# Performance work log

Hardware: AMD Instinct MI355X
Metric: run time of the kernel (lower is better)

Reference implementation:

```python
import jax, jax.numpy as jnp
import numpy as np

N, E, G = 50000, 1600000, 500
H, F, NG, L, OUT = 128, 128, 50, 6, 1
LOG2 = float(np.log(2.0))

def ssp(x):
    return jax.nn.softplus(x) - LOG2

def setup_inputs() -> dict:
    key = jax.random.key(0)
    ks = jax.random.split(key, 16)
    inp = {
        'z': jax.random.randint(ks[0], (N,), 0, 100),
        'pos': jax.random.normal(ks[1], (N, 3), jnp.float32) * 5.0,
        'batch': jnp.sort(jax.random.randint(ks[2], (N,), 0, G)),
        'edge_index': jax.random.randint(ks[3], (2, E), 0, N),
        # parameters
        'emb': jax.random.normal(ks[4], (100, H), jnp.float32) * 0.1,
        'dist_W': jax.random.normal(ks[5], (1, NG), jnp.float32) * 0.1,
        'dist_b': jnp.zeros((NG,), jnp.float32),
        'Wn': jax.random.normal(ks[6], (L, H, F), jnp.float32) * (1.0 / np.sqrt(H)),
        'We': jax.random.normal(ks[7], (L, NG, F), jnp.float32) * (1.0 / np.sqrt(NG)),
        'be': jnp.zeros((L, F), jnp.float32),
        'Wo': jax.random.normal(ks[8], (L, F, H), jnp.float32) * (1.0 / np.sqrt(F)),
        'bo': jnp.zeros((L, H), jnp.float32),
        'W1': jax.random.normal(ks[9], (H, H // 2), jnp.float32) * (1.0 / np.sqrt(H)),
        'b1': jnp.zeros((H // 2,), jnp.float32),
        'W2': jax.random.normal(ks[10], (H // 2, OUT), jnp.float32) * (1.0 / np.sqrt(H // 2)),
        'b2': jnp.zeros((OUT,), jnp.float32),
    }
    return inp

def reference(z, pos, batch, edge_index, emb, dist_W, dist_b, Wn, We, be, Wo, bo, W1, b1, W2, b2):
    row, col = edge_index[0], edge_index[1]
    # edge distances -> Linear(1, num_gaussians)
    dist = jnp.linalg.norm(pos[row] - pos[col], axis=-1)            # [E]
    e = dist[:, None] * dist_W[0][None, :] + dist_b                 # [E, NG]
    v = emb[z]                                                      # [N, H]
    # edge-conditioned message passing x num_layers
    for i in range(Wn.shape[0]):
        h = v @ Wn[i]                                               # [N, F]
        msg = h[col] * (e @ We[i] + be[i])                          # [E, F]
        agg = jax.ops.segment_sum(msg, row, num_segments=v.shape[0])
        v = ssp(agg @ Wo[i] + bo[i])                                # [N, H]
    # readout
    u = ssp(v @ W1 + b1) @ W2 + b2                                  # [N, OUT]
    return jax.ops.segment_sum(u, batch, num_segments=G)            # [G, OUT]
```

## Files before the change

### kernel.cpp

```cpp
#include <hip/hip_runtime.h>
#include <math.h>

#define HDIM 128
#define NGAUSS 50
#define NLAYER 6
#define TSTR 136
#define DINV (1.0f/512.0f)
#define NXCD 8
#define NSTRIPE 512

typedef unsigned short ushortT;
typedef __attribute__((ext_vector_type(8))) short bf16x8;
typedef __attribute__((ext_vector_type(4))) float f32x4;

static __device__ __forceinline__ float bf2f(unsigned short u){
  union { unsigned int i; float f; } x; x.i = ((unsigned int)u) << 16; return x.f;
}
static __device__ __forceinline__ float bitsf(unsigned int i){
  union { unsigned int i; float f; } x; x.i = i; return x.f;
}
static __device__ __forceinline__ unsigned short f2bf(float f){
  union { float f; unsigned int i; } x; x.f = f;
  unsigned int i = x.i;
  unsigned int r = (i + 0x7FFFu + ((i >> 16) & 1u)) >> 16;
  return (unsigned short)r;
}
static __device__ __forceinline__ float ssp(float x){
  return fmaxf(x, 0.0f) + __logf(1.0f + __expf(-fabsf(x))) - 0.69314718055994530942f;
}
static __device__ __forceinline__ f32x4 mfma4r(const bf16x8* a, const bf16x8* b){
  f32x4 d = {0.f, 0.f, 0.f, 0.f};
  d = __builtin_amdgcn_mfma_f32_16x16x32_bf16(a[0], b[0], d, 0, 0, 0);
  d = __builtin_amdgcn_mfma_f32_16x16x32_bf16(a[1], b[1], d, 0, 0, 0);
  d = __builtin_amdgcn_mfma_f32_16x16x32_bf16(a[2], b[2], d, 0, 0, 0);
  d = __builtin_amdgcn_mfma_f32_16x16x32_bf16(a[3], b[3], d, 0, 0, 0);
  return d;
}


__global__ __launch_bounds__(256)
void k_hist(const int* __restrict__ erow, int* __restrict__ hist,
            int E, int NB, int shift, int estripe){
  __shared__ int lh[512];
  int tid = threadIdx.x, w = blockIdx.x;
  for (int i = tid; i < NB; i += 256) lh[i] = 0;
  __syncthreads();
  int beg = w * estripe;
  int end = beg + estripe; if (end > E) end = E;
  for (int e = beg + tid; e < end; e += 256)
    atomicAdd(&lh[erow[e] >> shift], 1);
  __syncthreads();
  for (int i = tid; i < NB; i += 256) hist[w * 512 + i] = lh[i];
}

__global__ __launch_bounds__(256)
void k_colscan(int* __restrict__ hist, int* __restrict__ colTotal, int NB){
  __shared__ int sA[512], sB[512];
  int b = blockIdx.x, tid = threadIdx.x;
  sA[tid]       = hist[tid * 512 + b];
  sA[tid + 256] = hist[(tid + 256) * 512 + b];
  __syncthreads();
  int* pa = sA; int* pb = sB;
  for (int off = 1; off < 512; off <<= 1){
    for (int i = tid; i < 512; i += 256)
      pb[i] = pa[i] + (i >= off ? pa[i - off] : 0);
    __syncthreads();
    int* t = pa; pa = pb; pb = t;
  }
  int e0 = (tid == 0) ? 0 : pa[tid - 1];
  int e1 = pa[tid + 255];
  hist[tid * 512 + b]       = e0;
  hist[(tid + 256) * 512 + b] = e1;
  if (tid == 0) colTotal[b] = pa[511];
}

__global__ __launch_bounds__(256)
void k_bscan(const int* __restrict__ colTotal, int* __restrict__ bucketBase, int NB){
  __shared__ int sA[512], sB[512];
  int tid = threadIdx.x;
  for (int i = tid; i < 512; i += 256) sA[i] = (i < NB) ? colTotal[i] : 0;
  __syncthreads();
  int* pa = sA; int* pb = sB;
  for (int off = 1; off < 512; off <<= 1){
    for (int i = tid; i < 512; i += 256)
      pb[i] = pa[i] + (i >= off ? pa[i - off] : 0);
    __syncthreads();
    int* t = pa; pa = pb; pb = t;
  }
  for (int i = tid; i < NB; i += 256)
    bucketBase[i] = (i == 0) ? 0 : pa[i - 1];
  if (tid == 0) bucketBase[NB] = pa[NB - 1];
}

__global__ __launch_bounds__(256)
void k_scatter(const int* __restrict__ erow, const int* __restrict__ ecol,
               const float* __restrict__ pos, const int* __restrict__ hist,
               const int* __restrict__ bucketBase, uint2* __restrict__ stg,
               int E, int NB, int shift, int estripe){
  __shared__ int cur[512];
  int tid = threadIdx.x, w = blockIdx.x;
  for (int b = tid; b < NB; b += 256)
    cur[b] = bucketBase[b] + hist[w * 512 + b];
  __syncthreads();
  int beg = w * estripe;
  int end = beg + estripe; if (end > E) end = E;
  int mask = (1 << shift) - 1;
  for (int e = beg + tid; e < end; e += 256){
    int r = erow[e], c = ecol[e];
    float dx = pos[r*3+0] - pos[c*3+0];
    float dy = pos[r*3+1] - pos[c*3+1];
    float dz = pos[r*3+2] - pos[c*3+2];
    float d = sqrtf(dx*dx + dy*dy + dz*dz);
    int du = (int)(d * 512.0f + 0.5f);
    if (du > 65535) du = 65535;
    int p = atomicAdd(&cur[r >> shift], 1);
    uint2 t;
    t.x = ((unsigned int)c << 16) | (unsigned int)du;
    t.y = (unsigned int)(r & mask);
    stg[p] = t;
  }
}

__global__ __launch_bounds__(256)
void k_place(const uint2* __restrict__ stg, const int* __restrict__ bucketBase,
             int* __restrict__ offsets, unsigned int* __restrict__ csr,
             int N, int NB, int shift, int E){
  __shared__ int rc[1024];
  __shared__ int sA[1024], sB[1024];
  int b = blockIdx.x, tid = threadIdx.x;
  int R = 1 << shift;
  int r0 = b << shift;
  int s = bucketBase[b], e2 = bucketBase[b + 1];
  for (int i = tid; i < R; i += 256) rc[i] = 0;
  __syncthreads();
  for (int j = s + tid; j < e2; j += 256)
    atomicAdd(&rc[stg[j].y], 1);
  __syncthreads();
  for (int i = tid; i < R; i += 256) sA[i] = rc[i];
  __syncthreads();
  int* pa = sA; int* pb = sB;
  for (int off = 1; off < R; off <<= 1){
    for (int i = tid; i < R; i += 256)
      pb[i] = pa[i] + (i >= off ? pa[i - off] : 0);
    __syncthreads();
    int* t = pa; pa = pb; pb = t;
  }
  for (int i = tid; i < R; i += 256){
    int excl = (i == 0) ? 0 : pa[i - 1];
    rc[i] = excl;
    int r = r0 + i;
    if (r < N) offsets[r] = s + excl;
  }
  if (b == NB - 1 && tid == 0) offsets[N] = E;
  __syncthreads();
  for (int j = s + tid; j < e2; j += 256){
    uint2 t = stg[j];
    int slot = s + atomicAdd(&rc[t.y], 1);
    csr[slot] = t.x;
  }
}

__global__ void k_setup(const int* __restrict__ z, const float* __restrict__ emb,
                        ushortT* __restrict__ vhi,
                        const float* __restrict__ Wn, ushortT* __restrict__ WnT,
                        const float* __restrict__ Wo, ushortT* __restrict__ WoT,
                        const float* __restrict__ dW, const float* __restrict__ db,
                        const float* __restrict__ We, const float* __restrict__ be,
                        float* __restrict__ a, float* __restrict__ c,
                        const int* __restrict__ batch, int* __restrict__ groupOff,
                        const float* __restrict__ W1, ushortT* __restrict__ W1T,
                        int N, int G, int B1, int B2, int B4, int B5, int B7){
  int b = blockIdx.x;
  int tid = threadIdx.x;
  if (b < B1){
    int idx = b * 256 + tid;
    if (idx < N * HDIM){
      int n = idx >> 7, f = idx & 127;
      vhi[idx] = f2bf(emb[z[n] * HDIM + f]);
    }
    return;
  }
  b -= B1;
  if (b < B2){
    int idx = b * 256 + tid;
    if (idx < NLAYER * HDIM * HDIM){
      int mat = idx >> 14, rem = idx & 16383;
      int n = rem >> 7, k = rem & 127;
      WnT[idx] = f2bf(Wn[(mat << 14) + k * HDIM + n]);
    }
    return;
  }
  b -= B2;
  if (b < B2){
    int idx = b * 256 + tid;
    if (idx < NLAYER * HDIM * HDIM){
      int mat = idx >> 14, rem = idx & 16383;
      int n = rem >> 7, k = rem & 127;
      WoT[idx] = f2bf(Wo[(mat << 14) + k * HDIM + n]);
    }
    return;
  }
  b -= B2;
  if (b < B4){
    int idx = b * 256 + tid;
    if (idx < NLAYER * HDIM){
      int l = idx >> 7, f = idx & 127;
      float av = 0.f, cv = 0.f;
      for (int g = 0; g < NGAUSS; ++g){
        float we = We[(l * NGAUSS + g) * HDIM + f];
        av += dW[g] * we;
        cv += db[g] * we;
      }
      a[idx] = av;
      c[idx] = cv + be[idx];
    }
    return;
  }
  b -= B4;
  if (b < B5){
    int i = b * 256 + tid;
    if (i >= N) return;
    int bb = batch[i];
    if (i == 0){
      for (int g = 0; g <= bb; ++g) groupOff[g] = 0;
    } else {
      int pb = batch[i - 1];
      for (int g = pb + 1; g <= bb; ++g) groupOff[g] = i;
    }
    if (i == N - 1){
      for (int g = bb + 1; g <= G; ++g) groupOff[g] = N;
    }
    return;
  }
  b -= B5;
  if (b < B7){
    int idx = b * 256 + tid;
    if (idx < 64 * HDIM){
      int ncol = idx >> 7, k = idx & 127;
      W1T[idx] = f2bf(W1[k * 64 + ncol]);
    }
  }
}

__global__ __launch_bounds__(128, 2)
void k_gemm0(const ushortT* __restrict__ X, const ushortT* __restrict__ WT,
             ushortT* __restrict__ outHi, int N){
  int tid = threadIdx.x;
  int wave = tid >> 6, lane = tid & 63;
  int m = lane & 15, quad = lane >> 4;
  int ntiles = (N + 15) >> 4;
  int t0 = (blockIdx.x * 2 + wave) * 2;
  if (t0 >= ntiles) return;

  bf16x8 av[2][4];
  #pragma unroll
  for (int rt = 0; rt < 2; ++rt){
    int row = (t0 + rt) * 16 + m; if (row >= N) row = N - 1;
    #pragma unroll
    for (int kk = 0; kk < 4; ++kk)
      av[rt][kk] = *(const bf16x8*)(X + ((size_t)row << 7) + kk*32 + quad*8);
  }
  #pragma unroll
  for (int ct = 0; ct < 8; ++ct){
    int ncol = ct * 16 + m;
    const ushortT* bp = WT + ((size_t)ncol << 7) + quad*8;
    bf16x8 bb[4];
    #pragma unroll
    for (int kk = 0; kk < 4; ++kk) bb[kk] = *(const bf16x8*)(bp + kk*32);
    #pragma unroll
    for (int rt = 0; rt < 2; ++rt){
      f32x4 d = mfma4r(av[rt], bb);
      #pragma unroll
      for (int r = 0; r < 4; ++r){
        int orow = (t0 + rt) * 16 + quad*4 + r;
        if (orow < N) outHi[((size_t)orow << 7) + ncol] = f2bf(d[r]);
      }
    }
  }
}

#define AGG_PROC(P, DD) do { \
    unsigned int w_; float lo_, hi_; \
    w_ = (P).x; lo_ = bitsf(w_ << 16); hi_ = bitsf(w_ & 0xFFFF0000u); \
    s1[0] = fmaf(lo_, (DD), s1[0]); s0[0] += lo_; \
    s1[1] = fmaf(hi_, (DD), s1[1]); s0[1] += hi_; \
    w_ = (P).y; lo_ = bitsf(w_ << 16); hi_ = bitsf(w_ & 0xFFFF0000u); \
    s1[2] = fmaf(lo_, (DD), s1[2]); s0[2] += lo_; \
    s1[3] = fmaf(hi_, (DD), s1[3]); s0[3] += hi_; \
    w_ = (P).z; lo_ = bitsf(w_ << 16); hi_ = bitsf(w_ & 0xFFFF0000u); \
    s1[4] = fmaf(lo_, (DD), s1[4]); s0[4] += lo_; \
    s1[5] = fmaf(hi_, (DD), s1[5]); s0[5] += hi_; \
    w_ = (P).w; lo_ = bitsf(w_ << 16); hi_ = bitsf(w_ & 0xFFFF0000u); \
    s1[6] = fmaf(lo_, (DD), s1[6]); s0[6] += lo_; \
    s1[7] = fmaf(hi_, (DD), s1[7]); s0[7] += hi_; \
  } while(0)

#define GATH(Q) (*(const uint4*)(h + ((size_t)((Q) >> 16) << 7) + fl))

__global__ __launch_bounds__(256, 6)
void k_agg2(const ushortT* __restrict__ h, const int* __restrict__ offsets,
            const unsigned int* __restrict__ cd, const float* __restrict__ a,
            const float* __restrict__ c, ushortT* __restrict__ aggHi,
            int N, int segNodes){
  int xcd = blockIdx.x & (NXCD - 1);
  int idx = blockIdx.x >> 3;
  int node = xcd * segNodes + idx * 4 + (threadIdx.x >> 6);
  if (node >= N || node >= (xcd + 1) * segNodes) return;
  int lane = threadIdx.x & 63;
  int quarter = lane >> 4;
  int fl = (lane & 15) * 8;
  int s = offsets[node], e = offsets[node + 1];
  float s0[8] = {0.f,0.f,0.f,0.f,0.f,0.f,0.f,0.f};
  float s1[8] = {0.f,0.f,0.f,0.f,0.f,0.f,0.f,0.f};
  int efull = s + ((e - s) & ~7);
  int L = s;
  if (efull - s >= 16){
    unsigned int qA0 = cd[L + quarter],      qA1 = cd[L + 4 + quarter];
    uint4 pA0 = GATH(qA0), pA1 = GATH(qA1);
    unsigned int qB0 = cd[L + 8 + quarter],  qB1 = cd[L + 12 + quarter];
    uint4 pB0 = GATH(qB0), pB1 = GATH(qB1);
    float dA0 = (float)(qA0 & 0xFFFFu) * DINV, dA1 = (float)(qA1 & 0xFFFFu) * DINV;
    float dB0 = (float)(qB0 & 0xFFFFu) * DINV, dB1 = (float)(qB1 & 0xFFFFu) * DINV;
    L += 16;
    for (; L + 16 <= efull; L += 16){
      unsigned int nA0 = cd[L + quarter], nA1 = cd[L + 4 + quarter];
      AGG_PROC(pA0, dA0); AGG_PROC(pA1, dA1);
      pA0 = GATH(nA0); pA1 = GATH(nA1);
      dA0 = (float)(nA0 & 0xFFFFu) * DINV; dA1 = (float)(nA1 & 0xFFFFu) * DINV;
      unsigned int nB0 = cd[L + 8 + quarter], nB1 = cd[L + 12 + quarter];
      AGG_PROC(pB0, dB0); AGG_PROC(pB1, dB1);
      pB0 = GATH(nB0); pB1 = GATH(nB1);
      dB0 = (float)(nB0 & 0xFFFFu) * DINV; dB1 = (float)(nB1 & 0xFFFFu) * DINV;
    }
    AGG_PROC(pA0, dA0); AGG_PROC(pA1, dA1);
    AGG_PROC(pB0, dB0); AGG_PROC(pB1, dB1);
  }
  for (; L + 8 <= efull; L += 8){
    unsigned int q0 = cd[L + quarter], q1 = cd[L + 4 + quarter];
    uint4 p0 = GATH(q0), p1 = GATH(q1);
    float d0 = (float)(q0 & 0xFFFFu) * DINV, d1 = (float)(q1 & 0xFFFFu) * DINV;
    AGG_PROC(p0, d0); AGG_PROC(p1, d1);
  }
  for (int j = efull; j < e; j += 4){
    int myj = j + quarter;
    if (myj < e){
      unsigned int q = cd[myj];
      uint4 p = GATH(q);
      float dd = (float)(q & 0xFFFFu) * DINV;
      AGG_PROC(p, dd);
    }
  }
  float4 av0 = *(const float4*)(a + fl);
  float4 av1 = *(const float4*)(a + fl + 4);
  float4 cv0 = *(const float4*)(c + fl);
  float4 cv1 = *(const float4*)(c + fl + 4);
  float r[8];
  r[0] = av0.x * s1[0] + cv0.x * s0[0];
  r[1] = av0.y * s1[1] + cv0.y * s0[1];
  r[2] = av0.z * s1[2] + cv0.z * s0[2];
  r[3] = av0.w * s1[3] + cv0.w * s0[3];
  r[4] = av1.x * s1[4] + cv1.x * s0[4];
  r[5] = av1.y * s1[5] + cv1.y * s0[5];
  r[6] = av1.z * s1[6] + cv1.z * s0[6];
  r[7] = av1.w * s1[7] + cv1.w * s0[7];
  #pragma unroll
  for (int k = 0; k < 8; ++k){
    r[k] += __shfl_down(r[k], 32, 64);
    r[k] += __shfl_down(r[k], 16, 64);
  }
  if (quarter == 0){
    uint4 st;
    st.x = (unsigned int)f2bf(r[0]) | ((unsigned int)f2bf(r[1]) << 16);
    st.y = (unsigned int)f2bf(r[2]) | ((unsigned int)f2bf(r[3]) << 16);
    st.z = (unsigned int)f2bf(r[4]) | ((unsigned int)f2bf(r[5]) << 16);
    st.w = (unsigned int)f2bf(r[6]) | ((unsigned int)f2bf(r[7]) << 16);
    *(uint4*)(aggHi + ((size_t)node << 7) + fl) = st;
  }
}

__global__ __launch_bounds__(128, 2)
void k_fpair(const ushortT* __restrict__ agg, const ushortT* __restrict__ WoT,
             const float* __restrict__ bo, const ushortT* __restrict__ WnT,
             ushortT* __restrict__ outH, int N, int segTiles){
  __shared__ ushortT vt[2][32 * TSTR];
  int tid = threadIdx.x;
  int wave = tid >> 6, lane = tid & 63;
  int m = lane & 15, quad = lane >> 4;
  int ntiles = (N + 15) >> 4;
  int xcd = blockIdx.x & (NXCD - 1);
  int idx = blockIdx.x >> 3;
  int wjIdx = idx * 2 + wave;
  int segWJ = segTiles >> 1;
  if (wjIdx >= segWJ) return;
  int t0 = xcd * segTiles + wjIdx * 2;
  if (t0 >= ntiles) return;
  ushortT* vw = vt[wave];

  bf16x8 av[2][4];
  #pragma unroll
  for (int rt = 0; rt < 2; ++rt){
    int row = (t0 + rt) * 16 + m; if (row >= N) row = N - 1;
    #pragma unroll
    for (int kk = 0; kk < 4; ++kk)
      av[rt][kk] = *(const bf16x8*)(agg + ((size_t)row << 7) + kk*32 + quad*8);
  }
  #pragma unroll
  for (int ct = 0; ct < 8; ++ct){
    int ncol = ct * 16 + m;
    const ushortT* bp = WoT + ((size_t)ncol << 7) + quad*8;
    bf16x8 bb[4];
    #pragma unroll
    for (int kk = 0; kk < 4; ++kk) bb[kk] = *(const bf16x8*)(bp + kk*32);
    float bbias = bo[ncol];
    #pragma unroll
    for (int rt = 0; rt < 2; ++rt){
      f32x4 d = mfma4r(av[rt], bb);
      #pragma unroll
      for (int r = 0; r < 4; ++r)
        vw[(rt*16 + quad*4 + r) * TSTR + ncol] = f2bf(ssp(d[r] + bbias));
    }
  }
  bf16x8 a2[2][4];
  #pragma unroll
  for (int rt = 0; rt < 2; ++rt){
    #pragma unroll
    for (int kk = 0; kk < 4; ++kk)
      a2[rt][kk] = *(const bf16x8*)(&vw[(rt*16 + m) * TSTR + kk*32 + quad*8]);
  }
  #pragma unroll
  for (int ct = 0; ct < 8; ++ct){
    int ncol = ct * 16 + m;
    const ushortT* bp = WnT + ((size_t)ncol << 7) + quad*8;
    bf16x8 bb[4];
    #pragma unroll
    for (int kk = 0; kk < 4; ++kk) bb[kk] = *(const bf16x8*)(bp + kk*32);
    #pragma unroll
    for (int rt = 0; rt < 2; ++rt){
      f32x4 d = mfma4r(a2[rt], bb);
      #pragma unroll
      for (int r = 0; r < 4; ++r){
        int orow = (t0 + rt) * 16 + quad*4 + r;
        if (orow < N) outH[((size_t)orow << 7) + ncol] = f2bf(d[r]);
      }
    }
  }
}

__global__ __launch_bounds__(128, 2)
void k_gfinal(const ushortT* __restrict__ agg, const ushortT* __restrict__ WoT,
              const float* __restrict__ bo, const ushortT* __restrict__ W1T,
              const float* __restrict__ b1, const float* __restrict__ W2,
              const float* __restrict__ b2, float* __restrict__ u,
              int N, int segTiles){
  __shared__ ushortT vt[2][32 * TSTR];
  int tid = threadIdx.x;
  int wave = tid >> 6, lane = tid & 63;
  int m = lane & 15, quad = lane >> 4;
  int ntiles = (N + 15) >> 4;
  int xcd = blockIdx.x & (NXCD - 1);
  int idx = blockIdx.x >> 3;
  int wjIdx = idx * 2 + wave;
  int segWJ = segTiles >> 1;
  if (wjIdx >= segWJ) return;
  int t0 = xcd * segTiles + wjIdx * 2;
  if (t0 >= ntiles) return;
  ushortT* vw = vt[wave];

  bf16x8 av[2][4];
  #pragma unroll
  for (int rt = 0; rt < 2; ++rt){
    int row = (t0 + rt) * 16 + m; if (row >= N) row = N - 1;
    #pragma unroll
    for (int kk = 0; kk < 4; ++kk)
      av[rt][kk] = *(const bf16x8*)(agg + ((size_t)row << 7) + kk*32 + quad*8);
  }
  #pragma unroll
  for (int ct = 0; ct < 8; ++ct){
    int ncol = ct * 16 + m;
    const ushortT* bp = WoT + ((size_t)ncol << 7) + quad*8;
    bf16x8 bb[4];
    #pragma unroll
    for (int kk = 0; kk < 4; ++kk) bb[kk] = *(const bf16x8*)(bp + kk*32);
    float bbias = bo[ncol];
    #pragma unroll
    for (int rt = 0; rt < 2; ++rt){
      f32x4 d = mfma4r(av[rt], bb);
      #pragma unroll
      for (int r = 0; r < 4; ++r)
        vw[(rt*16 + quad*4 + r) * TSTR + ncol] = f2bf(ssp(d[r] + bbias));
    }
  }
  bf16x8 a2[2][4];
  #pragma unroll
  for (int rt = 0; rt < 2; ++rt){
    #pragma unroll
    for (int kk = 0; kk < 4; ++kk)
      a2[rt][kk] = *(const bf16x8*)(&vw[(rt*16 + m) * TSTR + kk*32 + quad*8]);
  }
  float acc[2][4] = {{0.f,0.f,0.f,0.f},{0.f,0.f,0.f,0.f}};
  #pragma unroll
  for (int ct = 0; ct < 4; ++ct){
    int ncol = ct * 16 + m;
    const ushortT* bp = W1T + ((size_t)ncol << 7) + quad*8;
    bf16x8 bb[4];
    #pragma unroll
    for (int kk = 0; kk < 4; ++kk) bb[kk] = *(const bf16x8*)(bp + kk*32);
    float bb1 = b1[ncol];
    float w2  = W2[ncol];
    #pragma unroll
    for (int rt = 0; rt < 2; ++rt){
      f32x4 d = mfma4r(a2[rt], bb);
      #pragma unroll
      for (int r = 0; r < 4; ++r)
        acc[rt][r] += ssp(d[r] + bb1) * w2;
    }
  }
  float bb2 = b2[0];
  #pragma unroll
  for (int rt = 0; rt < 2; ++rt){
    #pragma unroll
    for (int r = 0; r < 4; ++r){
      float v = acc[rt][r];
      v += __shfl_xor(v, 1, 64);
      v += __shfl_xor(v, 2, 64);
      v += __shfl_xor(v, 4, 64);
      v += __shfl_xor(v, 8, 64);
      if (m == 0){
        int orow = (t0 + rt) * 16 + quad*4 + r;
        if (orow < N) u[orow] = v + bb2;
      }
    }
  }
}

__global__ void k_gsum(const float* __restrict__ u, const int* __restrict__ groupOff,
                       float* __restrict__ out, int G){
  int g = blockIdx.x * 4 + (threadIdx.x >> 6);
  if (g >= G) return;
  int lane = threadIdx.x & 63;
  int s = groupOff[g], e = groupOff[g + 1];
  float acc = 0.f;
  for (int j = s + lane; j < e; j += 64) acc += u[j];
  #pragma unroll
  for (int off = 32; off > 0; off >>= 1)
    acc += __shfl_down(acc, off, 64);
  if (lane == 0) out[g] = acc;
}

extern "C" void kernel_launch(void* const* d_in, const int* in_sizes, int n_in,
                              void* d_out, int out_size, void* d_ws, size_t ws_size,
                              hipStream_t stream){
  const int N = in_sizes[0];
  const int E = in_sizes[3] / 2;
  const int G = out_size;

  const int*   z     = (const int*)d_in[0];
  const float* pos   = (const float*)d_in[1];
  const int*   batch = (const int*)d_in[2];
  const int*   eidx  = (const int*)d_in[3];
  const int*   erow  = eidx;
  const int*   ecol  = eidx + E;
  const float* emb   = (const float*)d_in[4];
  const float* dW    = (const float*)d_in[5];
  const float* db    = (const float*)d_in[6];
  const float* Wn    = (const float*)d_in[7];
  const float* We    = (const float*)d_in[8];
  const float* be    = (const float*)d_in[9];
  const float* Wo    = (const float*)d_in[10];
  const float* bo    = (const float*)d_in[11];
  const float* W1    = (const float*)d_in[12];
  const float* b1    = (const float*)d_in[13];
  const float* W2    = (const float*)d_in[14];
  const float* b2    = (const float*)d_in[15];

  char* ws = (char*)d_ws;
  size_t off = 0;
  auto alloc = [&](size_t bytes) -> char* {
    char* p = ws + off;
    off = (off + bytes + 255) & ~(size_t)255;
    return p;
  };
  size_t hbytes = (size_t)N * HDIM * 2;
  size_t stgbytes = (size_t)E * 8;
  int*          offsets  = (int*)         alloc((size_t)(N + 1) * 4);
  unsigned int* csr      = (unsigned int*)alloc((size_t)E * 4);
  ushortT*      h0       = (ushortT*)     alloc(hbytes);
  ushortT*      h1       = (ushortT*)     alloc(hbytes);
  ushortT*      vhi      = (ushortT*)     alloc(hbytes);
  ushortT*      agghi    = (ushortT*)     alloc(hbytes);
  ushortT*      stgbuf   = (ushortT*)     alloc(stgbytes);
  ushortT*      WnT      = (ushortT*)     alloc((size_t)NLAYER * HDIM * HDIM * 2);
  ushortT*      WoT      = (ushortT*)     alloc((size_t)NLAYER * HDIM * HDIM * 2);
  ushortT*      W1T      = (ushortT*)     alloc((size_t)64 * HDIM * 2);
  float*        a        = (float*)       alloc((size_t)NLAYER * HDIM * 4);
  float*        c        = (float*)       alloc((size_t)NLAYER * HDIM * 4);
  float*        u        = (float*)       alloc((size_t)N * 4);
  int*          groupOff = (int*)         alloc((size_t)(G + 1) * 4);

  int*   hist       = (int*)h1;
  int*   colTotal   = hist + NSTRIPE * 512;
  int*   bucketBase = colTotal + 512;
  uint2* stg        = (uint2*)stgbuf;

  int shift = 7;
  while ((((N - 1) >> shift) + 1) > 512) ++shift;
  int NB = ((N - 1) >> shift) + 1;
  int estripe = (E + NSTRIPE - 1) / NSTRIPE;

  int B1 = (N * HDIM + 255) / 256;
  int B2 = (NLAYER * HDIM * HDIM + 255) / 256;
  int B4 = (NLAYER * HDIM + 255) / 256;
  int B5 = (N + 255) / 256;
  int B7 = (64 * HDIM + 255) / 256;
  k_setup<<<B1 + 2*B2 + B4 + B5 + B7, 256, 0, stream>>>(
      z, emb, vhi, Wn, WnT, Wo, WoT,
      dW, db, We, be, a, c, batch, groupOff, W1, W1T,
      N, G, B1, B2, B4, B5, B7);

  k_hist   <<<NSTRIPE, 256, 0, stream>>>(erow, hist, E, NB, shift, estripe);
  k_colscan<<<NB,      256, 0, stream>>>(hist, colTotal, NB);
  k_bscan  <<<1,       256, 0, stream>>>(colTotal, bucketBase, NB);
  k_scatter<<<NSTRIPE, 256, 0, stream>>>(erow, ecol, pos, hist, bucketBase,
                                         stg, E, NB, shift, estripe);
  k_place  <<<NB,      256, 0, stream>>>(stg, bucketBase, offsets, csr, N, NB, shift, E);

  int ntiles = (N + 15) >> 4;
  int segTiles = (((ntiles + NXCD - 1) / NXCD) + 1) & ~1;
  int segNodes = segTiles * 16;
  int segWJ = segTiles >> 1;
  int aggGrid  = NXCD * ((segNodes + 3) / 4);
  int gGrid    = NXCD * ((segWJ + 1) / 2);
  int nwj = (ntiles + 1) / 2;
  int pairGrid = (nwj + 1) / 2;
  k_gemm0<<<pairGrid, 128, 0, stream>>>(vhi, WnT, h0, N);

  for (int l = 0; l < NLAYER; ++l){
    size_t wo = (size_t)l * HDIM * HDIM;
    const ushortT* hin  = (l & 1) ? h1 : h0;
    ushortT*       hout = (l & 1) ? h0 : h1;
    k_agg2<<<aggGrid, 256, 0, stream>>>(hin, offsets, csr,
                                        a + l * HDIM, c + l * HDIM, agghi, N, segNodes);
    if (l < NLAYER - 1){
      size_t wn = (size_t)(l + 1) * HDIM * HDIM;
      k_fpair<<<gGrid, 128, 0, stream>>>(agghi, WoT + wo, bo + (size_t)l * HDIM,
                                         WnT + wn, hout, N, segTiles);
    } else {
      k_gfinal<<<gGrid, 128, 0, stream>>>(agghi, WoT + wo, bo + (size_t)l * HDIM,
                                          W1T, b1, W2, b2, u, N, segTiles);
    }
  }
  k_gsum<<<(G + 3) / 4, 256, 0, stream>>>(u, groupOff, (float*)d_out, G);
}
```

Baseline: 579.8 us.

## Split node-GEMM column tiles across two waves per tile pair with block sync

The fused Wo/Wn (and final readout) kernels now use 256 threads per block, with two waves cooperating on each 32-row tile pair, each computing half of the output columns. A __syncthreads is added so both halves of the intermediate ssp activations are written to shared memory before the second GEMM reads full rows. In the final kernel, the partial readout sums from the two halves are combined through shared memory. This doubles the number of waves working on these kernels to improve latency hiding, at the cost of block-wide barriers and more per-block register pressure.

```diff
diff --git a/kernel.cpp b/kernel.cpp
--- a/kernel.cpp
+++ b/kernel.cpp
@@ -378,157 +378,174 @@
   }
 }
 
-__global__ __launch_bounds__(128, 2)
+__global__ __launch_bounds__(256, 2)
 void k_fpair(const ushortT* __restrict__ agg, const ushortT* __restrict__ WoT,
              const float* __restrict__ bo, const ushortT* __restrict__ WnT,
              ushortT* __restrict__ outH, int N, int segTiles){
   __shared__ ushortT vt[2][32 * TSTR];
   int tid = threadIdx.x;
   int wave = tid >> 6, lane = tid & 63;
+  int pairI = wave >> 1, half = wave & 1;
   int m = lane & 15, quad = lane >> 4;
   int ntiles = (N + 15) >> 4;
   int xcd = blockIdx.x & (NXCD - 1);
   int idx = blockIdx.x >> 3;
-  int wjIdx = idx * 2 + wave;
+  int wjIdx = idx * 2 + pairI;
   int segWJ = segTiles >> 1;
-  if (wjIdx >= segWJ) return;
   int t0 = xcd * segTiles + wjIdx * 2;
-  if (t0 >= ntiles) return;
-  ushortT* vw = vt[wave];
+  bool act = (wjIdx < segWJ) && (t0 < ntiles);
+  ushortT* vw = vt[pairI];
 
   bf16x8 av[2][4];
-  #pragma unroll
-  for (int rt = 0; rt < 2; ++rt){
-    int row = (t0 + rt) * 16 + m; if (row >= N) row = N - 1;
-    #pragma unroll
-    for (int kk = 0; kk < 4; ++kk)
-      av[rt][kk] = *(const bf16x8*)(agg + ((size_t)row << 7) + kk*32 + quad*8);
-  }
-  #pragma unroll
-  for (int ct = 0; ct < 8; ++ct){
-    int ncol = ct * 16 + m;
-    const ushortT* bp = WoT + ((size_t)ncol << 7) + quad*8;
-    bf16x8 bb[4];
-    #pragma unroll
-    for (int kk = 0; kk < 4; ++kk) bb[kk] = *(const bf16x8*)(bp + kk*32);
-    float bbias = bo[ncol];
+  if (act){
     #pragma unroll
     for (int rt = 0; rt < 2; ++rt){
-      f32x4 d = mfma4r(av[rt], bb);
-      #pragma unroll
-      for (int r = 0; r < 4; ++r)
-        vw[(rt*16 + quad*4 + r) * TSTR + ncol] = f2bf(ssp(d[r] + bbias));
-    }
-  }
-  bf16x8 a2[2][4];
-  #pragma unroll
-  for (int rt = 0; rt < 2; ++rt){
-    #pragma unroll
-    for (int kk = 0; kk < 4; ++kk)
-      a2[rt][kk] = *(const bf16x8*)(&vw[(rt*16 + m) * TSTR + kk*32 + quad*8]);
-  }
-  #pragma unroll
-  for (int ct = 0; ct < 8; ++ct){
-    int ncol = ct * 16 + m;
-    const ushortT* bp = WnT + ((size_t)ncol << 7) + quad*8;
-    bf16x8 bb[4];
-    #pragma unroll
-    for (int kk = 0; kk < 4; ++kk) bb[kk] = *(const bf16x8*)(bp + kk*32);
+      int row = (t0 + rt) * 16 + m; if (row >= N) row = N - 1;
+      #pragma unroll
+      for (int kk = 0; kk < 4; ++kk)
+        av[rt][kk] = *(const bf16x8*)(agg + ((size_t)row << 7) + kk*32 + quad*8);
+    }
+    #pragma unroll
+    for (int cti = 0; cti < 4; ++cti){
+      int ncol = (half * 4 + cti) * 16 + m;
+      const ushortT* bp = WoT + ((size_t)ncol << 7) + quad*8;
+      bf16x8 bb[4];
+      #pragma unroll
+      for (int kk = 0; kk < 4; ++kk) bb[kk] = *(const bf16x8*)(bp + kk*32);
+      float bbias = bo[ncol];
+      #pragma unroll
+      for (int rt = 0; rt < 2; ++rt){
+        f32x4 d = mfma4r(av[rt], bb);
+        #pragma unroll
+        for (int r = 0; r < 4; ++r)
+          vw[(rt*16 + quad*4 + r) * TSTR + ncol] = f2bf(ssp(d[r] + bbias));
+      }
+    }
+  }
+  __syncthreads();
+  if (act){
+    bf16x8 a2[2][4];
     #pragma unroll
     for (int rt = 0; rt < 2; ++rt){
-      f32x4 d = mfma4r(a2[rt], bb);
-      #pragma unroll
-      for (int r = 0; r < 4; ++r){
-        int orow = (t0 + rt) * 16 + quad*4 + r;
-        if (orow < N) outH[((size_t)orow << 7) + ncol] = f2bf(d[r]);
+      #pragma unroll
+      for (int kk = 0; kk < 4; ++kk)
+        a2[rt][kk] = *(const bf16x8*)(&vw[(rt*16 + m) * TSTR + kk*32 + quad*8]);
+    }
+    #pragma unroll
+    for (int cti = 0; cti < 4; ++cti){
+      int ncol = (half * 4 + cti) * 16 + m;
+      const ushortT* bp = WnT + ((size_t)ncol << 7) + quad*8;
+      bf16x8 bb[4];
+      #pragma unroll
+      for (int kk = 0; kk < 4; ++kk) bb[kk] = *(const bf16x8*)(bp + kk*32);
+      #pragma unroll
+      for (int rt = 0; rt < 2; ++rt){
+        f32x4 d = mfma4r(a2[rt], bb);
+        #pragma unroll
+        for (int r = 0; r < 4; ++r){
+          int orow = (t0 + rt) * 16 + quad*4 + r;
+          if (orow < N) outH[((size_t)orow << 7) + ncol] = f2bf(d[r]);
+        }
       }
     }
   }
 }
 
-__global__ __launch_bounds__(128, 2)
+__global__ __launch_bounds__(256, 2)
 void k_gfinal(const ushortT* __restrict__ agg, const ushortT* __restrict__ WoT,
               const float* __restrict__ bo, const ushortT* __restrict__ W1T,
               const float* __restrict__ b1, const float* __restrict__ W2,
               const float* __restrict__ b2, float* __restrict__ u,
               int N, int segTiles){
   __shared__ ushortT vt[2][32 * TSTR];
+  __shared__ float part[2][2][32];
   int tid = threadIdx.x;
   int wave = tid >> 6, lane = tid & 63;
+  int pairI = wave >> 1, half = wave & 1;
   int m = lane & 15, quad = lane >> 4;
   int ntiles = (N + 15) >> 4;
   int xcd = blockIdx.x & (NXCD - 1);
   int idx = blockIdx.x >> 3;
-  int wjIdx = idx * 2 + wave;
+  int wjIdx = idx * 2 + pairI;
   int segWJ = segTiles >> 1;
-  if (wjIdx >= segWJ) return;
   int t0 = xcd * segTiles + wjIdx * 2;
-  if (t0 >= ntiles) return;
-  ushortT* vw = vt[wave];
-
-  bf16x8 av[2][4];
-  #pragma unroll
-  for (int rt = 0; rt < 2; ++rt){
-    int row = (t0 + rt) * 16 + m; if (row >= N) row = N - 1;
-    #pragma unroll
-    for (int kk = 0; kk < 4; ++kk)
-      av[rt][kk] = *(const bf16x8*)(agg + ((size_t)row << 7) + kk*32 + quad*8);
-  }
-  #pragma unroll
-  for (int ct = 0; ct < 8; ++ct){
-    int ncol = ct * 16 + m;
-    const ushortT* bp = WoT + ((size_t)ncol << 7) + quad*8;
-    bf16x8 bb[4];
-    #pragma unroll
-    for (int kk = 0; kk < 4; ++kk) bb[kk] = *(const bf16x8*)(bp + kk*32);
-    float bbias = bo[ncol];
+  bool act = (wjIdx < segWJ) && (t0 < ntiles);
+  ushortT* vw = vt[pairI];
+
+  if (act){
+    bf16x8 av[2][4];
     #pragma unroll
     for (int rt = 0; rt < 2; ++rt){
-      f32x4 d = mfma4r(av[rt], bb);
-      #pragma unroll
-      for (int r = 0; r < 4; ++r)
-        vw[(rt*16 + quad*4 + r) * TSTR + ncol] = f2bf(ssp(d[r] + bbias));
-    }
-  }
-  bf16x8 a2[2][4];
-  #pragma unroll
-  for (int rt = 0; rt < 2; ++rt){
-    #pragma unroll
-    for (int kk = 0; kk < 4; ++kk)
-      a2[rt][kk] = *(const bf16x8*)(&vw[(rt*16 + m) * TSTR + kk*32 + quad*8]);
-  }
-  float acc[2][4] = {{0.f,0.f,0.f,0.f},{0.f,0.f,0.f,0.f}};
-  #pragma unroll
-  for (int ct = 0; ct < 4; ++ct){
-    int ncol = ct * 16 + m;
-    const ushortT* bp = W1T + ((size_t)ncol << 7) + quad*8;
-    bf16x8 bb[4];
-    #pragma unroll
-    for (int kk = 0; kk < 4; ++kk) bb[kk] = *(const bf16x8*)(bp + kk*32);
-    float bb1 = b1[ncol];
-    float w2  = W2[ncol];
+      int row = (t0 + rt) * 16 + m; if (row >= N) row = N - 1;
+      #pragma unroll
+      for (int kk = 0; kk < 4; ++kk)
+        av[rt][kk] = *(const bf16x8*)(agg + ((size_t)row << 7) + kk*32 + quad*8);
+    }
+    #pragma unroll
+    for (int cti = 0; cti < 4; ++cti){
+      int ncol = (half * 4 + cti) * 16 + m;
+      const ushortT* bp = WoT + ((size_t)ncol << 7) + quad*8;
+      bf16x8 bb[4];
+      #pragma unroll
+      for (int kk = 0; kk < 4; ++kk) bb[kk] = *(const bf16x8*)(bp + kk*32);
+      float bbias = bo[ncol];
+      #pragma unroll
+      for (int rt = 0; rt < 2; ++rt){
+        f32x4 d = mfma4r(av[rt], bb);
+        #pragma unroll
+        for (int r = 0; r < 4; ++r)
+          vw[(rt*16 + quad*4 + r) * TSTR + ncol] = f2bf(ssp(d[r] + bbias));
+      }
+    }
+  }
+  __syncthreads();
+  if (act){
+    bf16x8 a2[2][4];
     #pragma unroll
     for (int rt = 0; rt < 2; ++rt){
-      f32x4 d = mfma4r(a2[rt], bb);
-      #pragma unroll
-      for (int r = 0; r < 4; ++r)
-        acc[rt][r] += ssp(d[r] + bb1) * w2;
-    }
-  }
-  float bb2 = b2[0];
-  #pragma unroll
-  for (int rt = 0; rt < 2; ++rt){
-    #pragma unroll
-    for (int r = 0; r < 4; ++r){
-      float v = acc[rt][r];
-      v += __shfl_xor(v, 1, 64);
-      v += __shfl_xor(v, 2, 64);
-      v += __shfl_xor(v, 4, 64);
-      v += __shfl_xor(v, 8, 64);
-      if (m == 0){
-        int orow = (t0 + rt) * 16 + quad*4 + r;
-        if (orow < N) u[orow] = v + bb2;
+      #pragma unroll
+      for (int kk = 0; kk < 4; ++kk)
+        a2[rt][kk] = *(const bf16x8*)(&vw[(rt*16 + m) * TSTR + kk*32 + quad*8]);
+    }
+    float acc[2][4] = {{0.f,0.f,0.f,0.f},{0.f,0.f,0.f,0.f}};
+    #pragma unroll
+    for (int cti = 0; cti < 2; ++cti){
+      int ncol = (half * 2 + cti) * 16 + m;
+      const ushortT* bp = W1T + ((size_t)ncol << 7) + quad*8;
+      bf16x8 bb[4];
+      #pragma unroll
+      for (int kk = 0; kk < 4; ++kk) bb[kk] = *(const bf16x8*)(bp + kk*32);
+      float bb1 = b1[ncol];
+      float w2  = W2[ncol];
+      #pragma unroll
+      for (int rt = 0; rt < 2; ++rt){
+        f32x4 d = mfma4r(a2[rt], bb);
+        #pragma unroll
+        for (int r = 0; r < 4; ++r)
+          acc[rt][r] += ssp(d[r] + bb1) * w2;
       }
+    }
+    #pragma unroll
+    for (int rt = 0; rt < 2; ++rt){
+      #pragma unroll
+      for (int r = 0; r < 4; ++r){
+        float v = acc[rt][r];
+        v += __shfl_xor(v, 1, 64);
+        v += __shfl_xor(v, 2, 64);
+        v += __shfl_xor(v, 4, 64);
+        v += __shfl_xor(v, 8, 64);
+        if (m == 0) part[pairI][half][rt*16 + quad*4 + r] = v;
+      }
+    }
+  }
+  __syncthreads();
+  if (tid < 64){
+    int p = tid >> 5, row = tid & 31;
+    int wj = idx * 2 + p;
+    int tt = xcd * segTiles + wj * 2;
+    if (wj < segWJ && tt < ntiles){
+      int orow = tt * 16 + row;
+      if (orow < N) u[orow] = part[p][0][row] + part[p][1][row] + b2[0];
     }
   }
 }
@@ -642,10 +659,10 @@
                                         a + l * HDIM, c + l * HDIM, agghi, N, segNodes);
     if (l < NLAYER - 1){
       size_t wn = (size_t)(l + 1) * HDIM * HDIM;
-      k_fpair<<<gGrid, 128, 0, stream>>>(agghi, WoT + wo, bo + (size_t)l * HDIM,
+      k_fpair<<<gGrid, 256, 0, stream>>>(agghi, WoT + wo, bo + (size_t)l * HDIM,
                                          WnT + wn, hout, N, segTiles);
     } else {
-      k_gfinal<<<gGrid, 128, 0, stream>>>(agghi, WoT + wo, bo + (size_t)l * HDIM,
+      k_gfinal<<<gGrid, 256, 0, stream>>>(agghi, WoT + wo, bo + (size_t)l * HDIM,
                                           W1T, b1, W2, b2, u, N, segTiles);
     }
   }
```

After: 582.5 us. About the same (+0.5%).
